# Kernel optimization log

Measured on AMD Instinct MI355X. Metric: run time of the kernel, lower is better.

## Reference

```python
import jax, jax.numpy as jnp
import numpy as np

B, C, H, W = 8, 256, 128, 128
K = 3                      # kernel_size
GC = 16                    # group_channels
G = C // GC                # groups = 16
RED = 4                    # reduction_ratio (hardcoded in module)
CR = C // RED              # 64
PAD = (K - 1) // 2


def setup_inputs() -> dict:
    key = jax.random.key(0)
    ks = jax.random.split(key, 8)
    s = 0.05
    return {
        "x":  jax.random.normal(ks[0], (B, C, H, W), dtype=jnp.float32),
        # conv1[0]: 1x1 Conv2d(C, C//4)
        "w1": jax.random.normal(ks[1], (CR, C), dtype=jnp.float32) * s,
        "b1": jax.random.normal(ks[2], (CR,), dtype=jnp.float32) * s,
        # conv1[1]: depthwise KxK Conv2d(C//4, C//4, groups=C//4), padding=K//2
        "wd": jax.random.normal(ks[3], (CR, 1, K, K), dtype=jnp.float32) * s,
        "bd": jax.random.normal(ks[4], (CR,), dtype=jnp.float32) * s,
        # conv2: 1x1 Conv2d(C//4, K*K*G)
        "w2": jax.random.normal(ks[5], (K * K * G, CR), dtype=jnp.float32) * s,
        "b2": jax.random.normal(ks[6], (K * K * G,), dtype=jnp.float32) * s,
    }


def _forward(x, w1, b1, wd, bd, w2, b2):
    # weight generation branch: 1x1 conv -> depthwise KxK conv -> 1x1 conv
    y = jnp.einsum("oc,bchw->bohw", w1, x) + b1[None, :, None, None]
    y = jax.lax.conv_general_dilated(
        y, wd, window_strides=(1, 1),
        padding=[(PAD, PAD), (PAD, PAD)],
        feature_group_count=CR,
        dimension_numbers=("NCHW", "OIHW", "NCHW"),
    ) + bd[None, :, None, None]
    w = jnp.einsum("oc,bchw->bohw", w2, y) + b2[None, :, None, None]
    w = w.reshape(B, G, K, K, H, W)  # per-pixel dynamic depthwise weights

    # involution-style per-pixel depthwise conv, stride=1, padding=(K-1)//2
    xr = x.reshape(B, G, GC, H, W)
    xp = jnp.pad(xr, ((0, 0), (0, 0), (0, 0), (PAD, PAD), (PAD, PAD)))
    out = jnp.zeros((B, G, GC, H, W), dtype=x.dtype)
    for kh in range(K):          # small fixed structural loop (K*K = 9 taps)
        for kw in range(K):
            out = out + xp[:, :, :, kh:kh + H, kw:kw + W] * w[:, :, kh, kw][:, :, None, :, :]
    return out.reshape(B, C, H, W)


def reference(x, w1, b1, wd, bd, w2, b2):
    return _forward(x, w1, b1, wd, bd, w2, b2)
```

## Files before the change

kernel.cpp:

```cpp
#include <hip/hip_runtime.h>
#include <hip/hip_bf16.h>

#define HW    16384
#define IMW   128
#define IMH   128
#define CIN   256
#define CR    64
#define G     16
#define GC    16
#define M2    144

typedef __attribute__((ext_vector_type(8))) short short8;
typedef __attribute__((ext_vector_type(4))) float floatx4;

static __device__ __forceinline__ short f2bf(float f) {
  union { float f; unsigned u; } v; v.f = f;
  unsigned r = v.u + 0x7fffu + ((v.u >> 16) & 1u);
  return (short)(r >> 16);
}
static __device__ __forceinline__ float bf2f(short s) {
  union { unsigned u; float f; } v; v.u = ((unsigned)(unsigned short)s) << 16;
  return v.f;
}

__global__ __launch_bounds__(256) void k_cvt(const float* __restrict__ w1,
                                             const float* __restrict__ w2,
                                             short* __restrict__ w1b,
                                             short* __restrict__ w2b,
                                             short* __restrict__ w2r) {
  const int blk = blockIdx.x;
  if (blk < 64) {
    const int i = blk * 256 + threadIdx.x;
    w1b[i] = f2bf(w1[i]);
  } else {
    const int i = (blk - 64) * 256 + threadIdx.x;
    const float v = w2[i];
    const short hb = f2bf(v);
    w2b[i] = hb;
    w2r[i] = f2bf(v - bf2f(hb));
  }
}

__global__ __launch_bounds__(256) void k_conv1_mfma(const float* __restrict__ x,
                                                    const short* __restrict__ w1b,
                                                    const float* __restrict__ b1,
                                                    short* __restrict__ y1b) {
  const int blk  = blockIdx.x;
  const int b    = blk >> 8;
  const int pt   = blk & 255;
  const int wave = threadIdx.x >> 6;
  const int lane = threadIdx.x & 63;
  const int quad = lane >> 4;
  const int l16  = lane & 15;
  const int p    = pt * 64 + wave * 16 + l16;

  const float* xb = x + (size_t)b * CIN * HW + p;

  floatx4 acc[4];
#pragma unroll
  for (int mt = 0; mt < 4; ++mt)
#pragma unroll
    for (int r = 0; r < 4; ++r) acc[mt][r] = b1[mt * 16 + quad * 4 + r];

#pragma unroll 1
  for (int kk = 0; kk < CIN; kk += 64) {
    short8 af0[4], af1[4];
#pragma unroll
    for (int mt = 0; mt < 4; ++mt) {
      af0[mt] = *(const short8*)(w1b + (mt * 16 + l16) * CIN + kk + quad * 8);
      af1[mt] = *(const short8*)(w1b + (mt * 16 + l16) * CIN + kk + 32 + quad * 8);
    }
    float xv0[8], xv1[8];
#pragma unroll
    for (int j = 0; j < 8; ++j)
      xv0[j] = xb[(size_t)(kk + quad * 8 + j) * HW];
#pragma unroll
    for (int j = 0; j < 8; ++j)
      xv1[j] = xb[(size_t)(kk + 32 + quad * 8 + j) * HW];

    short8 bf0, bf1;
#pragma unroll
    for (int j = 0; j < 8; ++j) bf0[j] = f2bf(xv0[j]);
#pragma unroll
    for (int j = 0; j < 8; ++j) bf1[j] = f2bf(xv1[j]);

#pragma unroll
    for (int mt = 0; mt < 4; ++mt)
      acc[mt] = __builtin_amdgcn_mfma_f32_16x16x32_bf16(af0[mt], bf0, acc[mt], 0, 0, 0);
#pragma unroll
    for (int mt = 0; mt < 4; ++mt)
      acc[mt] = __builtin_amdgcn_mfma_f32_16x16x32_bf16(af1[mt], bf1, acc[mt], 0, 0, 0);
  }

  short* yb = y1b + (size_t)b * CR * HW + p;
#pragma unroll
  for (int mt = 0; mt < 4; ++mt)
#pragma unroll
    for (int r = 0; r < 4; ++r)
      yb[(size_t)(mt * 16 + quad * 4 + r) * HW] = f2bf(acc[mt][r]);
}

__global__ __launch_bounds__(256) void k_dw(const short* __restrict__ y1b,
                                            const float* __restrict__ wd,
                                            const float* __restrict__ bd,
                                            short* __restrict__ y2b) {
  const int blk   = blockIdx.x;
  const int strip = blk & 3;
  const int c     = (blk >> 2) & 63;
  const int b     = blk >> 8;
  const int tcol  = threadIdx.x & 15;
  const int trow  = threadIdx.x >> 4;
  const int r0    = strip * 32 + trow * 2;
  const int c0    = tcol * 8;

  const short* src = y1b + (size_t)(b * CR + c) * HW;

  const float mcl = c0 > 0 ? 1.f : 0.f;
  const float mcr = c0 + 8 < IMW ? 1.f : 0.f;
  const int   cl  = c0 > 0 ? c0 - 1 : 0;
  const int   crr = c0 + 8 < IMW ? c0 + 8 : IMW - 1;

  float f[4][10];
#pragma unroll
  for (int i = 0; i < 4; ++i) {
    const int rr = r0 - 1 + i;
    const int rc = rr < 0 ? 0 : (rr > IMH - 1 ? IMH - 1 : rr);
    const float mr = (rr < 0 || rr > IMH - 1) ? 0.f : 1.f;
    const short* row = src + rc * IMW;
    const short8 v = *(const short8*)(row + c0);
#pragma unroll
    for (int j = 0; j < 8; ++j) f[i][j + 1] = mr * bf2f(v[j]);
    f[i][0] = mr * mcl * bf2f(row[cl]);
    f[i][9] = mr * mcr * bf2f(row[crr]);
  }

  float wv[9];
#pragma unroll
  for (int j = 0; j < 9; ++j) wv[j] = wd[c * 9 + j];
  const float bias = bd[c];

  short* dst = y2b + (size_t)(b * CR + c) * HW + r0 * IMW + c0;
#pragma unroll
  for (int i = 0; i < 2; ++i) {
    short8 o;
#pragma unroll
    for (int xcol = 0; xcol < 8; ++xcol) {
      float acc = bias;
#pragma unroll
      for (int kh = 0; kh < 3; ++kh)
#pragma unroll
        for (int kw = 0; kw < 3; ++kw)
          acc += wv[kh * 3 + kw] * f[i + kh][xcol + kw];
      o[xcol] = f2bf(acc);
    }
    *(short8*)(dst + i * IMW) = o;
  }
}

__global__ __launch_bounds__(256) void k_wgen_invol(const float* __restrict__ x,
                                                    const short* __restrict__ y2b,
                                                    const short* __restrict__ w2b,
                                                    const short* __restrict__ w2r,
                                                    const float* __restrict__ b2,
                                                    float* __restrict__ out) {
  __shared__ float wgt[M2 * 64];
  const int blk  = blockIdx.x;
  const int b    = blk >> 8;
  const int pt   = blk & 255;
  const int tid  = threadIdx.x;
  const int wave = tid >> 6;
  const int lane = tid & 63;
  const int quad = lane >> 4;
  const int l16  = lane & 15;

  {
    const int p = pt * 64 + wave * 16 + l16;
    const short* y2p = y2b + (size_t)b * CR * HW + p;

    floatx4 acc[9];
#pragma unroll
    for (int mt = 0; mt < 9; ++mt)
#pragma unroll
      for (int r = 0; r < 4; ++r) acc[mt][r] = b2[mt * 16 + quad * 4 + r];

#pragma unroll
    for (int kk = 0; kk < CR; kk += 32) {
      short8 bfrag;
#pragma unroll
      for (int j = 0; j < 8; ++j)
        bfrag[j] = y2p[(size_t)(kk + quad * 8 + j) * HW];
#pragma unroll
      for (int mt = 0; mt < 9; ++mt) {
        const short8 af = *(const short8*)(w2b + (mt * 16 + l16) * CR + kk + quad * 8);
        acc[mt] = __builtin_amdgcn_mfma_f32_16x16x32_bf16(af, bfrag, acc[mt], 0, 0, 0);
      }
#pragma unroll
      for (int mt = 0; mt < 9; ++mt) {
        const short8 ar = *(const short8*)(w2r + (mt * 16 + l16) * CR + kk + quad * 8);
        acc[mt] = __builtin_amdgcn_mfma_f32_16x16x32_bf16(ar, bfrag, acc[mt], 0, 0, 0);
      }
    }

#pragma unroll
    for (int mt = 0; mt < 9; ++mt)
#pragma unroll
      for (int r = 0; r < 4; ++r)
        wgt[(mt * 16 + quad * 4 + r) * 64 + wave * 16 + l16] = acc[mt][r];
  }
  __syncthreads();

  const int pq  = tid & 15;
  const int g   = tid >> 4;
  const int h   = pt >> 1;
  const int c0q = (pt & 1) * 64 + pq * 4;
  const int p0  = h * IMW + c0q;

  float wv[9][4];
#pragma unroll
  for (int j = 0; j < 9; ++j) {
    const float4 v = *(const float4*)&wgt[(g * 9 + j) * 64 + pq * 4];
    wv[j][0] = v.x; wv[j][1] = v.y; wv[j][2] = v.z; wv[j][3] = v.w;
  }

  if (h == 0) {
#pragma unroll
    for (int j = 0; j < 3; ++j)
      wv[j][0] = wv[j][1] = wv[j][2] = wv[j][3] = 0.f;
  }
  if (h == IMH - 1) {
#pragma unroll
    for (int j = 6; j < 9; ++j)
      wv[j][0] = wv[j][1] = wv[j][2] = wv[j][3] = 0.f;
  }
  if (c0q == 0)       { wv[0][0] = wv[3][0] = wv[6][0] = 0.f; }
  if (c0q == IMW - 4) { wv[2][3] = wv[5][3] = wv[8][3] = 0.f; }

  const int r[3] = { (h > 0 ? h - 1 : 0) * IMW, h * IMW,
                     (h < IMH - 1 ? h + 1 : IMH - 1) * IMW };
  const int cl = c0q > 0 ? c0q - 1 : 0;
  const int cr = c0q + 4 < IMW ? c0q + 4 : IMW - 1;

  const float* xg = x   + ((size_t)b * CIN + (size_t)g * GC) * HW;
  float*       og = out + ((size_t)b * CIN + (size_t)g * GC) * HW;

#pragma unroll 2
  for (int cc = 0; cc < GC; ++cc) {
    const float* xp = xg + (size_t)cc * HW;
    float v[3][6];
#pragma unroll
    for (int rr = 0; rr < 3; ++rr) {
      const float4 m = *(const float4*)(xp + r[rr] + c0q);
      v[rr][0] = xp[r[rr] + cl];
      v[rr][1] = m.x; v[rr][2] = m.y; v[rr][3] = m.z; v[rr][4] = m.w;
      v[rr][5] = xp[r[rr] + cr];
    }
    float o[4];
#pragma unroll
    for (int px = 0; px < 4; ++px) {
      float acc = 0.f;
#pragma unroll
      for (int kh = 0; kh < 3; ++kh)
#pragma unroll
        for (int kw = 0; kw < 3; ++kw)
          acc += wv[kh * 3 + kw][px] * v[kh][px + kw];
      o[px] = acc;
    }
    float4 ov; ov.x = o[0]; ov.y = o[1]; ov.z = o[2]; ov.w = o[3];
    *(float4*)(og + (size_t)cc * HW + p0) = ov;
  }
}

extern "C" void kernel_launch(void* const* d_in, const int* in_sizes, int n_in,
                              void* d_out, int out_size, void* d_ws, size_t ws_size,
                              hipStream_t stream) {
  const float* x  = (const float*)d_in[0];
  const float* w1 = (const float*)d_in[1];
  const float* b1 = (const float*)d_in[2];
  const float* wd = (const float*)d_in[3];
  const float* bd = (const float*)d_in[4];
  const float* w2 = (const float*)d_in[5];
  const float* b2 = (const float*)d_in[6];
  float* out = (float*)d_out;

  short* w2b = (short*)d_ws;
  short* w2r = (short*)((char*)d_ws + 18432);
  short* y1b = (short*)((char*)d_ws + 36864);
  short* y2b = (short*)((char*)d_ws + 16814080);
  short* w1b = y2b;

  k_cvt<<<dim3(100), dim3(256), 0, stream>>>(w1, w2, w1b, w2b, w2r);
  k_conv1_mfma<<<dim3(2048), dim3(256), 0, stream>>>(x, w1b, b1, y1b);
  k_dw<<<dim3(2048), dim3(256), 0, stream>>>(y1b, wd, bd, y2b);
  k_wgen_invol<<<dim3(2048), dim3(256), 0, stream>>>(x, y2b, w2b, w2r, b2, out);
}
```

Baseline: 403.4 us.

## Split weight-gen/involution by batch half and stage conv1 input via LDS

Conv1 now loads x tiles into LDS with global_load_lds and walks K in 32-wide steps. The fused weight-gen and involution kernel is split two ways. For batches 0-3, an MFMA kernel writes the dynamic weights to scratch (the upper half of the output buffer), and a separate involution kernel reads them back. For batches 4-7, a new FP32 scalar kernel computes the weights and applies the involution in one pass. The aim is to cut LDS pressure and occupancy limits in the fused kernel, at the cost of extra global traffic and more launches. The scratch reuse only works because batches 4-7 are written after the first half is finished.

```diff
diff --git a/kernel.cpp b/kernel.cpp
--- a/kernel.cpp
+++ b/kernel.cpp
@@ -22,6 +22,10 @@
   union { unsigned u; float f; } v; v.u = ((unsigned)(unsigned short)s) << 16;
   return v.f;
 }
+
+#define GLL16(g, l) __builtin_amdgcn_global_load_lds( \
+    (const __attribute__((address_space(1))) void*)(g), \
+    (__attribute__((address_space(3))) void*)(l), 16, 0, 0)
 
 __global__ __launch_bounds__(256) void k_cvt(const float* __restrict__ w1,
                                              const float* __restrict__ w2,
@@ -45,16 +49,21 @@
                                                     const short* __restrict__ w1b,
                                                     const float* __restrict__ b1,
                                                     short* __restrict__ y1b) {
+  __shared__ float xs[2048];
   const int blk  = blockIdx.x;
   const int b    = blk >> 8;
   const int pt   = blk & 255;
-  const int wave = threadIdx.x >> 6;
-  const int lane = threadIdx.x & 63;
+  const int tid  = threadIdx.x;
+  const int wave = tid >> 6;
+  const int lane = tid & 63;
   const int quad = lane >> 4;
   const int l16  = lane & 15;
-  const int p    = pt * 64 + wave * 16 + l16;
-
-  const float* xb = x + (size_t)b * CIN * HW + p;
+  const int px0  = pt * 64;
+  const int p    = px0 + wave * 16 + l16;
+
+  const float* xb = x + (size_t)b * CIN * HW + px0;
+  const int krow = tid >> 4;
+  const int scol = (tid & 15) * 4;
 
   floatx4 acc[4];
 #pragma unroll
@@ -63,33 +72,25 @@
     for (int r = 0; r < 4; ++r) acc[mt][r] = b1[mt * 16 + quad * 4 + r];
 
 #pragma unroll 1
-  for (int kk = 0; kk < CIN; kk += 64) {
-    short8 af0[4], af1[4];
-#pragma unroll
-    for (int mt = 0; mt < 4; ++mt) {
-      af0[mt] = *(const short8*)(w1b + (mt * 16 + l16) * CIN + kk + quad * 8);
-      af1[mt] = *(const short8*)(w1b + (mt * 16 + l16) * CIN + kk + 32 + quad * 8);
-    }
-    float xv0[8], xv1[8];
+  for (int kk = 0; kk < CIN; kk += 32) {
+    GLL16(xb + (size_t)(kk + krow) * HW + scol,      xs + wave * 256);
+    GLL16(xb + (size_t)(kk + 16 + krow) * HW + scol, xs + 1024 + wave * 256);
+    __syncthreads();
+
+    short8 af[4];
+#pragma unroll
+    for (int mt = 0; mt < 4; ++mt)
+      af[mt] = *(const short8*)(w1b + (mt * 16 + l16) * CIN + kk + quad * 8);
+
+    short8 bfrag;
 #pragma unroll
     for (int j = 0; j < 8; ++j)
-      xv0[j] = xb[(size_t)(kk + quad * 8 + j) * HW];
-#pragma unroll
-    for (int j = 0; j < 8; ++j)
-      xv1[j] = xb[(size_t)(kk + 32 + quad * 8 + j) * HW];
-
-    short8 bf0, bf1;
-#pragma unroll
-    for (int j = 0; j < 8; ++j) bf0[j] = f2bf(xv0[j]);
-#pragma unroll
-    for (int j = 0; j < 8; ++j) bf1[j] = f2bf(xv1[j]);
+      bfrag[j] = f2bf(xs[(quad * 8 + j) * 64 + wave * 16 + l16]);
 
 #pragma unroll
     for (int mt = 0; mt < 4; ++mt)
-      acc[mt] = __builtin_amdgcn_mfma_f32_16x16x32_bf16(af0[mt], bf0, acc[mt], 0, 0, 0);
-#pragma unroll
-    for (int mt = 0; mt < 4; ++mt)
-      acc[mt] = __builtin_amdgcn_mfma_f32_16x16x32_bf16(af1[mt], bf1, acc[mt], 0, 0, 0);
+      acc[mt] = __builtin_amdgcn_mfma_f32_16x16x32_bf16(af[mt], bfrag, acc[mt], 0, 0, 0);
+    __syncthreads();
   }
 
   short* yb = y1b + (size_t)b * CR * HW + p;
@@ -157,71 +158,74 @@
   }
 }
 
-__global__ __launch_bounds__(256) void k_wgen_invol(const float* __restrict__ x,
-                                                    const short* __restrict__ y2b,
-                                                    const short* __restrict__ w2b,
-                                                    const short* __restrict__ w2r,
-                                                    const float* __restrict__ b2,
-                                                    float* __restrict__ out) {
-  __shared__ float wgt[M2 * 64];
+__global__ __launch_bounds__(256) void k_wgen(const short* __restrict__ y2b,
+                                              const short* __restrict__ w2b,
+                                              const short* __restrict__ w2r,
+                                              const float* __restrict__ b2,
+                                              float* __restrict__ wdyn) {
   const int blk  = blockIdx.x;
   const int b    = blk >> 8;
   const int pt   = blk & 255;
-  const int tid  = threadIdx.x;
-  const int wave = tid >> 6;
-  const int lane = tid & 63;
+  const int wave = threadIdx.x >> 6;
+  const int lane = threadIdx.x & 63;
   const int quad = lane >> 4;
   const int l16  = lane & 15;
-
-  {
-    const int p = pt * 64 + wave * 16 + l16;
-    const short* y2p = y2b + (size_t)b * CR * HW + p;
-
-    floatx4 acc[9];
-#pragma unroll
-    for (int mt = 0; mt < 9; ++mt)
-#pragma unroll
-      for (int r = 0; r < 4; ++r) acc[mt][r] = b2[mt * 16 + quad * 4 + r];
-
-#pragma unroll
-    for (int kk = 0; kk < CR; kk += 32) {
-      short8 bfrag;
-#pragma unroll
-      for (int j = 0; j < 8; ++j)
-        bfrag[j] = y2p[(size_t)(kk + quad * 8 + j) * HW];
-#pragma unroll
-      for (int mt = 0; mt < 9; ++mt) {
-        const short8 af = *(const short8*)(w2b + (mt * 16 + l16) * CR + kk + quad * 8);
-        acc[mt] = __builtin_amdgcn_mfma_f32_16x16x32_bf16(af, bfrag, acc[mt], 0, 0, 0);
-      }
-#pragma unroll
-      for (int mt = 0; mt < 9; ++mt) {
-        const short8 ar = *(const short8*)(w2r + (mt * 16 + l16) * CR + kk + quad * 8);
-        acc[mt] = __builtin_amdgcn_mfma_f32_16x16x32_bf16(ar, bfrag, acc[mt], 0, 0, 0);
-      }
-    }
-
-#pragma unroll
-    for (int mt = 0; mt < 9; ++mt)
-#pragma unroll
-      for (int r = 0; r < 4; ++r)
-        wgt[(mt * 16 + quad * 4 + r) * 64 + wave * 16 + l16] = acc[mt][r];
-  }
-  __syncthreads();
-
-  const int pq  = tid & 15;
-  const int g   = tid >> 4;
-  const int h   = pt >> 1;
-  const int c0q = (pt & 1) * 64 + pq * 4;
-  const int p0  = h * IMW + c0q;
-
+  const int p    = pt * 64 + wave * 16 + l16;
+
+  const short* y2p = y2b + (size_t)b * CR * HW + p;
+
+  floatx4 acc[9];
+#pragma unroll
+  for (int mt = 0; mt < 9; ++mt)
+#pragma unroll
+    for (int r = 0; r < 4; ++r) acc[mt][r] = b2[mt * 16 + quad * 4 + r];
+
+#pragma unroll
+  for (int kk = 0; kk < CR; kk += 32) {
+    short8 bfrag;
+#pragma unroll
+    for (int j = 0; j < 8; ++j)
+      bfrag[j] = y2p[(size_t)(kk + quad * 8 + j) * HW];
+#pragma unroll
+    for (int mt = 0; mt < 9; ++mt) {
+      const short8 af = *(const short8*)(w2b + (mt * 16 + l16) * CR + kk + quad * 8);
+      acc[mt] = __builtin_amdgcn_mfma_f32_16x16x32_bf16(af, bfrag, acc[mt], 0, 0, 0);
+    }
+#pragma unroll
+    for (int mt = 0; mt < 9; ++mt) {
+      const short8 ar = *(const short8*)(w2r + (mt * 16 + l16) * CR + kk + quad * 8);
+      acc[mt] = __builtin_amdgcn_mfma_f32_16x16x32_bf16(ar, bfrag, acc[mt], 0, 0, 0);
+    }
+  }
+
+  float* wb = wdyn + (size_t)b * M2 * HW + p;
+#pragma unroll
+  for (int mt = 0; mt < 9; ++mt)
+#pragma unroll
+    for (int r = 0; r < 4; ++r)
+      wb[(size_t)(mt * 16 + quad * 4 + r) * HW] = acc[mt][r];
+}
+
+__global__ __launch_bounds__(256) void k_invol(const float* __restrict__ x,
+                                               const float* __restrict__ wdyn,
+                                               float* __restrict__ out) {
+  const int blk  = blockIdx.x;
+  const int s    = blk & 15;
+  const int g    = (blk >> 4) & 15;
+  const int b    = blk >> 8;
+  const int tcol = threadIdx.x & 31;
+  const int trow = threadIdx.x >> 5;
+  const int h    = s * 8 + trow;
+  const int c0   = tcol * 4;
+  const int p0   = h * IMW + c0;
+
+  const float* wp = wdyn + ((size_t)b * M2 + (size_t)g * 9) * HW + p0;
   float wv[9][4];
 #pragma unroll
   for (int j = 0; j < 9; ++j) {
-    const float4 v = *(const float4*)&wgt[(g * 9 + j) * 64 + pq * 4];
+    const float4 v = *(const float4*)(wp + (size_t)j * HW);
     wv[j][0] = v.x; wv[j][1] = v.y; wv[j][2] = v.z; wv[j][3] = v.w;
   }
-
   if (h == 0) {
 #pragma unroll
     for (int j = 0; j < 3; ++j)
@@ -232,13 +236,13 @@
     for (int j = 6; j < 9; ++j)
       wv[j][0] = wv[j][1] = wv[j][2] = wv[j][3] = 0.f;
   }
-  if (c0q == 0)       { wv[0][0] = wv[3][0] = wv[6][0] = 0.f; }
-  if (c0q == IMW - 4) { wv[2][3] = wv[5][3] = wv[8][3] = 0.f; }
+  if (c0 == 0)       { wv[0][0] = wv[3][0] = wv[6][0] = 0.f; }
+  if (c0 == IMW - 4) { wv[2][3] = wv[5][3] = wv[8][3] = 0.f; }
 
   const int r[3] = { (h > 0 ? h - 1 : 0) * IMW, h * IMW,
                      (h < IMH - 1 ? h + 1 : IMH - 1) * IMW };
-  const int cl = c0q > 0 ? c0q - 1 : 0;
-  const int cr = c0q + 4 < IMW ? c0q + 4 : IMW - 1;
+  const int cl = c0 > 0 ? c0 - 1 : 0;
+  const int cr = c0 + 4 < IMW ? c0 + 4 : IMW - 1;
 
   const float* xg = x   + ((size_t)b * CIN + (size_t)g * GC) * HW;
   float*       og = out + ((size_t)b * CIN + (size_t)g * GC) * HW;
@@ -249,7 +253,7 @@
     float v[3][6];
 #pragma unroll
     for (int rr = 0; rr < 3; ++rr) {
-      const float4 m = *(const float4*)(xp + r[rr] + c0q);
+      const float4 m = *(const float4*)(xp + r[rr] + c0);
       v[rr][0] = xp[r[rr] + cl];
       v[rr][1] = m.x; v[rr][2] = m.y; v[rr][3] = m.z; v[rr][4] = m.w;
       v[rr][5] = xp[r[rr] + cr];
@@ -267,6 +271,77 @@
     }
     float4 ov; ov.x = o[0]; ov.y = o[1]; ov.z = o[2]; ov.w = o[3];
     *(float4*)(og + (size_t)cc * HW + p0) = ov;
+  }
+}
+
+__global__ __launch_bounds__(256) void k_conv2invol(const float* __restrict__ x,
+                                                    const short* __restrict__ y2b,
+                                                    const float* __restrict__ w2,
+                                                    const float* __restrict__ b2,
+                                                    float* __restrict__ out) {
+  const int blk  = blockIdx.x;
+  const int tile = blk & 63;
+  const int gp   = (blk >> 6) & 7;
+  const int b    = 4 + (blk >> 9);
+  const int g0   = gp * 2;
+  const int tid  = threadIdx.x;
+  const int tr   = tid >> 5;
+  const int tc   = tid & 31;
+  const int h    = (tile >> 2) * 8 + tr;
+  const int w    = (tile & 3) * 32 + tc;
+  const int p    = h * IMW + w;
+
+  float wv[2][9];
+#pragma unroll
+  for (int q = 0; q < 2; ++q)
+#pragma unroll
+    for (int j = 0; j < 9; ++j) wv[q][j] = b2[(g0 + q) * 9 + j];
+
+  const short* y2p = y2b + (size_t)b * CR * HW + p;
+#pragma unroll 2
+  for (int c = 0; c < CR; c += 4) {
+    const float v0 = bf2f(y2p[(size_t)(c + 0) * HW]);
+    const float v1 = bf2f(y2p[(size_t)(c + 1) * HW]);
+    const float v2 = bf2f(y2p[(size_t)(c + 2) * HW]);
+    const float v3 = bf2f(y2p[(size_t)(c + 3) * HW]);
+#pragma unroll
+    for (int q = 0; q < 2; ++q)
+#pragma unroll
+      for (int j = 0; j < 9; ++j) {
+        const float4 wq = *(const float4*)(w2 + ((g0 + q) * 9 + j) * CR + c);
+        wv[q][j] += wq.x * v0 + wq.y * v1 + wq.z * v2 + wq.w * v3;
+      }
+  }
+
+  const int   hcl[3] = {h > 0 ? h - 1 : 0, h, h < IMH - 1 ? h + 1 : IMH - 1};
+  const int   wcl[3] = {w > 0 ? w - 1 : 0, w, w < IMW - 1 ? w + 1 : IMW - 1};
+  const float mr[3]  = {h > 0 ? 1.f : 0.f, 1.f, h < IMH - 1 ? 1.f : 0.f};
+  const float mc[3]  = {w > 0 ? 1.f : 0.f, 1.f, w < IMW - 1 ? 1.f : 0.f};
+  int rel[9];
+#pragma unroll
+  for (int kh = 0; kh < 3; ++kh)
+#pragma unroll
+    for (int kw = 0; kw < 3; ++kw) {
+      rel[kh * 3 + kw] = hcl[kh] * IMW + wcl[kw];
+      const float m = mr[kh] * mc[kw];
+      wv[0][kh * 3 + kw] *= m;
+      wv[1][kh * 3 + kw] *= m;
+    }
+
+  const float* xb = x + (size_t)b * CIN * HW;
+  float*       ob = out + (size_t)b * CIN * HW;
+
+#pragma unroll
+  for (int q = 0; q < 2; ++q) {
+#pragma unroll 4
+    for (int cc = 0; cc < GC; ++cc) {
+      const int ch = (g0 + q) * GC + cc;
+      const float* xp = xb + (size_t)ch * HW;
+      float acc = 0.f;
+#pragma unroll
+      for (int j = 0; j < 9; ++j) acc += wv[q][j] * xp[rel[j]];
+      ob[(size_t)ch * HW + p] = acc;
+    }
   }
 }
 
@@ -284,12 +359,16 @@
 
   short* w2b = (short*)d_ws;
   short* w2r = (short*)((char*)d_ws + 18432);
-  short* y1b = (short*)((char*)d_ws + 36864);
-  short* y2b = (short*)((char*)d_ws + 16814080);
+  short* y1b = (short*)((char*)d_ws + 65536);
+  short* y2b = (short*)((char*)d_ws + 65536 + 16777216);
   short* w1b = y2b;
+
+  float* wdyn = out + (size_t)4 * CIN * HW;
 
   k_cvt<<<dim3(100), dim3(256), 0, stream>>>(w1, w2, w1b, w2b, w2r);
   k_conv1_mfma<<<dim3(2048), dim3(256), 0, stream>>>(x, w1b, b1, y1b);
   k_dw<<<dim3(2048), dim3(256), 0, stream>>>(y1b, wd, bd, y2b);
-  k_wgen_invol<<<dim3(2048), dim3(256), 0, stream>>>(x, y2b, w2b, w2r, b2, out);
-}
+  k_wgen<<<dim3(1024), dim3(256), 0, stream>>>(y2b, w2b, w2r, b2, wdyn);
+  k_invol<<<dim3(1024), dim3(256), 0, stream>>>(x, wdyn, out);
+  k_conv2invol<<<dim3(2048), dim3(256), 0, stream>>>(x, y2b, w2, b2, out);
+}
```

After: 381.2 us. 1.06x faster.
